# Performance work log

Measured on AMD Instinct MI355X. Metric: run time of the kernel, lower is better.

Reference implementation:

```python
import jax
jax.config.update("jax_enable_x64", True)
import jax.numpy as jnp
import numpy as np

LEAF_VOXEL_SIZE = 0.1
SCALE_UP_FACTOR = 2.0
VOXEL_LEVEL_NUM = 4
BUFFER_SIZE = 4194304
FEATURE_DIM = 8
N_FEATURES = 500000
N_QUERY = 1000000
FEATURE_STD = 0.01

PRIMES = jnp.array([73856093, 19349669, 83492791], dtype=jnp.int64)
# 8 voxel-corner offsets, matching self.steps ordering (z fastest)
STEPS = jnp.array([[0,0,0],[0,0,1],[0,1,0],[0,1,1],[1,0,0],[1,0,1],[1,1,0],[1,1,1]], dtype=jnp.float32)


def setup_inputs() -> dict:
    key = jax.random.key(0)
    k1, k2, k3, k4 = jax.random.split(key, 4)
    # query points spread over a few meters of scene
    query_points = 5.0 * jax.random.normal(k1, (N_QUERY, 3), dtype=jnp.float32)
    features = FEATURE_STD * jax.random.normal(k2, (VOXEL_LEVEL_NUM, N_FEATURES, FEATURE_DIM), dtype=jnp.float32)
    idx = jax.random.randint(k3, (VOXEL_LEVEL_NUM, BUFFER_SIZE), 0, N_FEATURES, dtype=jnp.int64)
    empty = jax.random.uniform(k4, (VOXEL_LEVEL_NUM, BUFFER_SIZE)) < 0.05
    feature_indexs = jnp.where(empty, jnp.int64(-1), idx)
    return {"query_points": query_points, "features": features, "feature_indexs": feature_indexs}


def _interp_coeffs(q, vs):
    # trilinear weights in the same corner order as STEPS -> [N, 8]
    d = q / vs - jnp.floor(q / vs)           # [N,3]
    tx, ty, tz = d[:, 0], d[:, 1], d[:, 2]
    w = jnp.stack([
        (1-tx)*(1-ty)*(1-tz), (1-tx)*(1-ty)*tz, (1-tx)*ty*(1-tz), (1-tx)*ty*tz,
        tx*(1-ty)*(1-tz),     tx*(1-ty)*tz,     tx*ty*(1-tz),     tx*ty*tz,
    ], axis=-1)
    return w


def reference(query_points, features, feature_indexs):
    N = query_points.shape[0]
    sum_features = jnp.zeros((N, FEATURE_DIM), dtype=jnp.float32)
    valid_mask = jnp.ones((N,), dtype=bool)
    for i in range(VOXEL_LEVEL_NUM):
        vs = LEAF_VOXEL_SIZE * SCALE_UP_FACTOR ** i
        grids = jnp.floor(query_points / vs)                       # [N,3]
        corners = (grids[:, None, :] + STEPS).astype(jnp.int64)    # [N,8,3]
        keys = (corners * PRIMES).sum(-1) % BUFFER_SIZE            # [N,8]
        idx = feature_indexs[i][keys]                              # [N,8]
        mask = idx.min(axis=1) >= 0                                # [N]
        safe_idx = jnp.maximum(idx, 0)
        feats = features[i][safe_idx]                              # [N,8,D]
        coeffs = _interp_coeffs(query_points, vs)                  # [N,8]
        contrib = jnp.einsum('ncd,nc->nd', feats, coeffs)          # [N,D]
        sum_features = sum_features + jnp.where(mask[:, None], contrib, 0.0)
        if i == 0:
            valid_mask = mask
    return sum_features, valid_mask
```

## Files before the change

kernel.cpp:

```cpp
#include <hip/hip_runtime.h>

#define BUF_MASK 4194303u
#define BUF_SIZE 4194304
#define NFEAT 500000
#define FDIM 8
#define NLVL 4
#define NBINS 262144
#define NXCD 8

__global__ void detect_int64_kernel(const unsigned int* __restrict__ fi,
                                    int* __restrict__ flag) {
    if (blockIdx.x == 0 && threadIdx.x == 0) {
        int cnt = 0;
        for (int k = 0; k < 128; ++k) {
            unsigned int w = fi[2 * k + 1];
            cnt += (w == 0u || w == 0xFFFFFFFFu) ? 1 : 0;
        }
        *flag = (cnt >= 96) ? 1 : 0;
    }
}

__device__ __forceinline__ unsigned part3(unsigned x) {
    x &= 0x3FFu;
    x = (x | (x << 16)) & 0x030000FFu;
    x = (x | (x << 8))  & 0x0300F00Fu;
    x = (x | (x << 4))  & 0x030C30C3u;
    x = (x | (x << 2))  & 0x09249249u;
    return x;
}

__global__ __launch_bounds__(256) void bin_kernel(
    const float* __restrict__ qp, unsigned* __restrict__ hist,
    unsigned* __restrict__ binA, unsigned* __restrict__ rankA, int N)
{
    int i = blockIdx.x * blockDim.x + threadIdx.x;
    if (i >= N) return;
    float x = qp[3 * (size_t)i + 0];
    float y = qp[3 * (size_t)i + 1];
    float z = qp[3 * (size_t)i + 2];
    int cx = (int)floorf(x * 1.25f) + 32;
    int cy = (int)floorf(y * 1.25f) + 32;
    int cz = (int)floorf(z * 1.25f) + 32;
    cx = min(max(cx, 0), 63); cy = min(max(cy, 0), 63); cz = min(max(cz, 0), 63);
    unsigned m = (part3((unsigned)cx) << 2) | (part3((unsigned)cy) << 1) | part3((unsigned)cz);
    unsigned r = atomicAdd(&hist[m], 1u);
    binA[i] = m; rankA[i] = r;
}

__global__ __launch_bounds__(512) void scan_block(
    const unsigned* __restrict__ hist, unsigned* __restrict__ starts,
    unsigned* __restrict__ bsum)
{
    __shared__ unsigned tmp[512];
    int b = blockIdx.x, t = threadIdx.x;
    unsigned v = hist[(size_t)b * 512 + t];
    tmp[t] = v; __syncthreads();
    for (int o = 1; o < 512; o <<= 1) {
        unsigned add = (t >= o) ? tmp[t - o] : 0u;
        __syncthreads();
        tmp[t] += add;
        __syncthreads();
    }
    starts[(size_t)b * 512 + t] = tmp[t] - v;
    if (t == 511) bsum[b] = tmp[t];
}

__global__ __launch_bounds__(512) void scan_sums(unsigned* __restrict__ bsum) {
    __shared__ unsigned tmp[512];
    int t = threadIdx.x;
    unsigned v = bsum[t];
    tmp[t] = v; __syncthreads();
    for (int o = 1; o < 512; o <<= 1) {
        unsigned add = (t >= o) ? tmp[t - o] : 0u;
        __syncthreads();
        tmp[t] += add;
        __syncthreads();
    }
    bsum[t] = tmp[t] - v;
}

__global__ __launch_bounds__(512) void scan_add(
    unsigned* __restrict__ starts, const unsigned* __restrict__ bsum)
{
    starts[(size_t)blockIdx.x * 512 + threadIdx.x] += bsum[blockIdx.x];
}

__global__ __launch_bounds__(256) void scatter_kernel(
    const float* __restrict__ qp, const unsigned* __restrict__ binA,
    const unsigned* __restrict__ rankA, const unsigned* __restrict__ starts,
    float4* __restrict__ sorted, int N)
{
    int i = blockIdx.x * blockDim.x + threadIdx.x;
    if (i >= N) return;
    unsigned pos = starts[binA[i]] + rankA[i];
    sorted[pos] = make_float4(qp[3 * (size_t)i + 0], qp[3 * (size_t)i + 1],
                              qp[3 * (size_t)i + 2], __uint_as_float((unsigned)i));
}

__global__ __launch_bounds__(256) void nvh_sorted_kernel(
    const float4* __restrict__ sq,
    const float* __restrict__ feats,
    const int*   __restrict__ fidx,
    const int*   __restrict__ flagp,
    float* __restrict__ out,
    int N)
{
    unsigned nwg = gridDim.x, b = blockIdx.x;
    unsigned q = nwg / NXCD, r = nwg % NXCD;
    unsigned xcd = b % NXCD, off = b / NXCD;
    unsigned swz = (xcd < r ? xcd * (q + 1) : r * (q + 1) + (xcd - r) * q) + off;
    int i = (int)(swz * blockDim.x + threadIdx.x);
    if (i >= N) return;
    const int shift = *flagp;

    float4 qv = sq[i];
    float qx = qv.x, qy = qv.y, qz = qv.z;
    unsigned orig = __float_as_uint(qv.w);

    float frx[NLVL], fry[NLVL], frz[NLVL];
    int   idxs[NLVL][8];

    #pragma unroll
    for (int l = 0; l < NLVL; ++l) {
        const float vs = 0.1f * (float)(1 << l);
        float tx = qx / vs, ty = qy / vs, tz = qz / vs;
        float gx = floorf(tx), gy = floorf(ty), gz = floorf(tz);
        frx[l] = tx - gx; fry[l] = ty - gy; frz[l] = tz - gz;
        unsigned h = (unsigned)(int)gx * 73856093u
                   + (unsigned)(int)gy * 19349669u
                   + (unsigned)(int)gz * 83492791u;
        const int* base = fidx + (((size_t)l * BUF_SIZE) << shift);
        #pragma unroll
        for (int c = 0; c < 8; ++c) {
            unsigned key = h;
            if (c & 4) key += 73856093u;
            if (c & 2) key += 19349669u;
            if (c & 1) key += 83492791u;
            key &= BUF_MASK;
            idxs[l][c] = base[(size_t)key << shift];
        }
    }

    float acc[8] = {0.f, 0.f, 0.f, 0.f, 0.f, 0.f, 0.f, 0.f};
    float maskv = 0.0f;

    #pragma unroll
    for (int l = 0; l < NLVL; ++l) {
        int mn = idxs[l][0];
        #pragma unroll
        for (int c = 1; c < 8; ++c) mn = min(mn, idxs[l][c]);
        bool valid = (mn >= 0);
        if (l == 0) maskv = valid ? 1.0f : 0.0f;
        if (valid) {
            const float* fb = feats + (size_t)l * (size_t)NFEAT * FDIM;
            float tx = frx[l], ty = fry[l], tz = frz[l];
            float sx[2] = {1.0f - tx, tx};
            float sy[2] = {1.0f - ty, ty};
            float sz[2] = {1.0f - tz, tz};
            #pragma unroll
            for (int c = 0; c < 8; ++c) {
                float w = (sx[(c >> 2) & 1] * sy[(c >> 1) & 1]) * sz[c & 1];
                const float4* f4 = (const float4*)(fb + (size_t)idxs[l][c] * FDIM);
                float4 a = f4[0];
                float4 b2 = f4[1];
                acc[0] += w * a.x;  acc[1] += w * a.y;
                acc[2] += w * a.z;  acc[3] += w * a.w;
                acc[4] += w * b2.x; acc[5] += w * b2.y;
                acc[6] += w * b2.z; acc[7] += w * b2.w;
            }
        }
    }

    float4* o = (float4*)(out + (size_t)orig * 8);
    o[0] = make_float4(acc[0], acc[1], acc[2], acc[3]);
    o[1] = make_float4(acc[4], acc[5], acc[6], acc[7]);
    out[(size_t)8 * N + orig] = maskv;
}

__global__ __launch_bounds__(256) void nvh_kernel(
    const float* __restrict__ qp, const float* __restrict__ feats,
    const int* __restrict__ fidx, const int* __restrict__ flagp,
    float* __restrict__ out, int N)
{
    int i = blockIdx.x * blockDim.x + threadIdx.x;
    if (i >= N) return;
    const int shift = *flagp;
    float qx = qp[3 * (size_t)i + 0];
    float qy = qp[3 * (size_t)i + 1];
    float qz = qp[3 * (size_t)i + 2];
    float frx[NLVL], fry[NLVL], frz[NLVL];
    int   idxs[NLVL][8];
    #pragma unroll
    for (int l = 0; l < NLVL; ++l) {
        const float vs = 0.1f * (float)(1 << l);
        float tx = qx / vs, ty = qy / vs, tz = qz / vs;
        float gx = floorf(tx), gy = floorf(ty), gz = floorf(tz);
        frx[l] = tx - gx; fry[l] = ty - gy; frz[l] = tz - gz;
        unsigned h = (unsigned)(int)gx * 73856093u
                   + (unsigned)(int)gy * 19349669u
                   + (unsigned)(int)gz * 83492791u;
        const int* base = fidx + (((size_t)l * BUF_SIZE) << shift);
        #pragma unroll
        for (int c = 0; c < 8; ++c) {
            unsigned key = h;
            if (c & 4) key += 73856093u;
            if (c & 2) key += 19349669u;
            if (c & 1) key += 83492791u;
            key &= BUF_MASK;
            idxs[l][c] = base[(size_t)key << shift];
        }
    }
    float acc[8] = {0.f, 0.f, 0.f, 0.f, 0.f, 0.f, 0.f, 0.f};
    float maskv = 0.0f;
    #pragma unroll
    for (int l = 0; l < NLVL; ++l) {
        int mn = idxs[l][0];
        #pragma unroll
        for (int c = 1; c < 8; ++c) mn = min(mn, idxs[l][c]);
        bool valid = (mn >= 0);
        if (l == 0) maskv = valid ? 1.0f : 0.0f;
        if (valid) {
            const float* fb = feats + (size_t)l * (size_t)NFEAT * FDIM;
            float tx = frx[l], ty = fry[l], tz = frz[l];
            float sx[2] = {1.0f - tx, tx};
            float sy[2] = {1.0f - ty, ty};
            float sz[2] = {1.0f - tz, tz};
            #pragma unroll
            for (int c = 0; c < 8; ++c) {
                float w = (sx[(c >> 2) & 1] * sy[(c >> 1) & 1]) * sz[c & 1];
                const float4* f4 = (const float4*)(fb + (size_t)idxs[l][c] * FDIM);
                float4 a = f4[0];
                float4 b2 = f4[1];
                acc[0] += w * a.x;  acc[1] += w * a.y;
                acc[2] += w * a.z;  acc[3] += w * a.w;
                acc[4] += w * b2.x; acc[5] += w * b2.y;
                acc[6] += w * b2.z; acc[7] += w * b2.w;
            }
        }
    }
    float4* o = (float4*)(out + (size_t)i * 8);
    o[0] = make_float4(acc[0], acc[1], acc[2], acc[3]);
    o[1] = make_float4(acc[4], acc[5], acc[6], acc[7]);
    out[(size_t)8 * N + i] = maskv;
}

extern "C" void kernel_launch(void* const* d_in, const int* in_sizes, int n_in,
                              void* d_out, int out_size, void* d_ws, size_t ws_size,
                              hipStream_t stream) {
    const float* qp    = (const float*)d_in[0];
    const float* feats = (const float*)d_in[1];
    const int*   fidx  = (const int*)d_in[2];
    int N = in_sizes[0] / 3;
    int blocks = (N + 255) / 256;

    char* ws = (char*)d_ws;
    size_t off = 0;
    int*      flag   = (int*)(ws + off);      off += 256;
    unsigned* hist   = (unsigned*)(ws + off); off += (size_t)NBINS * 4;
    unsigned* starts = (unsigned*)(ws + off); off += (size_t)NBINS * 4;
    unsigned* bsum   = (unsigned*)(ws + off); off += 512 * 4;
    unsigned* binA   = (unsigned*)(ws + off); off += (size_t)N * 4;
    unsigned* rankA  = (unsigned*)(ws + off); off += (size_t)N * 4;
    off = (off + 15) & ~(size_t)15;
    float4*   sorted = (float4*)(ws + off);   off += (size_t)N * 16;

    detect_int64_kernel<<<1, 64, 0, stream>>>((const unsigned int*)d_in[2], flag);

    if (ws_size < off) {
        nvh_kernel<<<blocks, 256, 0, stream>>>(qp, feats, fidx, flag, (float*)d_out, N);
        return;
    }

    hipMemsetAsync(hist, 0, (size_t)NBINS * 4, stream);
    bin_kernel<<<blocks, 256, 0, stream>>>(qp, hist, binA, rankA, N);
    scan_block<<<512, 512, 0, stream>>>(hist, starts, bsum);
    scan_sums<<<1, 512, 0, stream>>>(bsum);
    scan_add<<<512, 512, 0, stream>>>(starts, bsum);
    scatter_kernel<<<blocks, 256, 0, stream>>>(qp, binA, rankA, starts, sorted, N);
    nvh_sorted_kernel<<<blocks, 256, 0, stream>>>(sorted, feats, fidx, flag, (float*)d_out, N);
}
```

Before: 373.0 us.

## Replace stored bin/rank arrays with atomic cursor scatter and nontemporal memory ops

The binning pass no longer writes per-point bin and rank arrays. The scatter pass recomputes the Morton bin and claims its slot through an atomic increment on a per-bin cursor copied from the exclusive scan. Query reads, sorted-buffer writes and output stores now use nontemporal loads and stores so they do not pollute the cache used by the random feature gathers. This removes about 8 MB of intermediate traffic, but adds a second round of 1M atomics and makes the order of points within a bin nondeterministic.

```diff
diff --git a/kernel.cpp b/kernel.cpp
--- a/kernel.cpp
+++ b/kernel.cpp
@@ -8,6 +8,8 @@
 #define NBINS 262144
 #define NXCD 8
 
+typedef float f4 __attribute__((ext_vector_type(4)));
+
 __global__ void detect_int64_kernel(const unsigned int* __restrict__ fi,
                                     int* __restrict__ flag) {
     if (blockIdx.x == 0 && threadIdx.x == 0) {
@@ -29,27 +31,28 @@
     return x;
 }
 
-__global__ __launch_bounds__(256) void bin_kernel(
-    const float* __restrict__ qp, unsigned* __restrict__ hist,
-    unsigned* __restrict__ binA, unsigned* __restrict__ rankA, int N)
-{
-    int i = blockIdx.x * blockDim.x + threadIdx.x;
-    if (i >= N) return;
-    float x = qp[3 * (size_t)i + 0];
-    float y = qp[3 * (size_t)i + 1];
-    float z = qp[3 * (size_t)i + 2];
+__device__ __forceinline__ unsigned morton_bin(float x, float y, float z) {
     int cx = (int)floorf(x * 1.25f) + 32;
     int cy = (int)floorf(y * 1.25f) + 32;
     int cz = (int)floorf(z * 1.25f) + 32;
     cx = min(max(cx, 0), 63); cy = min(max(cy, 0), 63); cz = min(max(cz, 0), 63);
-    unsigned m = (part3((unsigned)cx) << 2) | (part3((unsigned)cy) << 1) | part3((unsigned)cz);
-    unsigned r = atomicAdd(&hist[m], 1u);
-    binA[i] = m; rankA[i] = r;
+    return (part3((unsigned)cx) << 2) | (part3((unsigned)cy) << 1) | part3((unsigned)cz);
+}
+
+__global__ __launch_bounds__(256) void hist_kernel(
+    const float* __restrict__ qp, unsigned* __restrict__ hist, int N)
+{
+    int i = blockIdx.x * blockDim.x + threadIdx.x;
+    if (i >= N) return;
+    float x = __builtin_nontemporal_load(qp + 3 * (size_t)i + 0);
+    float y = __builtin_nontemporal_load(qp + 3 * (size_t)i + 1);
+    float z = __builtin_nontemporal_load(qp + 3 * (size_t)i + 2);
+    atomicAdd(&hist[morton_bin(x, y, z)], 1u);
 }
 
 __global__ __launch_bounds__(512) void scan_block(
     const unsigned* __restrict__ hist, unsigned* __restrict__ starts,
-    unsigned* __restrict__ bsum)
+    unsigned* __restrict__ cursor, unsigned* __restrict__ bsum)
 {
     __shared__ unsigned tmp[512];
     int b = blockIdx.x, t = threadIdx.x;
@@ -61,7 +64,9 @@
         tmp[t] += add;
         __syncthreads();
     }
-    starts[(size_t)b * 512 + t] = tmp[t] - v;
+    unsigned ex = tmp[t] - v;
+    starts[(size_t)b * 512 + t] = ex;
+    cursor[(size_t)b * 512 + t] = ex;
     if (t == 511) bsum[b] = tmp[t];
 }
 
@@ -80,25 +85,32 @@
 }
 
 __global__ __launch_bounds__(512) void scan_add(
-    unsigned* __restrict__ starts, const unsigned* __restrict__ bsum)
-{
-    starts[(size_t)blockIdx.x * 512 + threadIdx.x] += bsum[blockIdx.x];
+    unsigned* __restrict__ starts, unsigned* __restrict__ cursor,
+    const unsigned* __restrict__ bsum)
+{
+    unsigned add = bsum[blockIdx.x];
+    size_t p = (size_t)blockIdx.x * 512 + threadIdx.x;
+    starts[p] += add;
+    cursor[p] += add;
 }
 
 __global__ __launch_bounds__(256) void scatter_kernel(
-    const float* __restrict__ qp, const unsigned* __restrict__ binA,
-    const unsigned* __restrict__ rankA, const unsigned* __restrict__ starts,
-    float4* __restrict__ sorted, int N)
+    const float* __restrict__ qp, unsigned* __restrict__ cursor,
+    f4* __restrict__ sorted, int N)
 {
     int i = blockIdx.x * blockDim.x + threadIdx.x;
     if (i >= N) return;
-    unsigned pos = starts[binA[i]] + rankA[i];
-    sorted[pos] = make_float4(qp[3 * (size_t)i + 0], qp[3 * (size_t)i + 1],
-                              qp[3 * (size_t)i + 2], __uint_as_float((unsigned)i));
+    float x = __builtin_nontemporal_load(qp + 3 * (size_t)i + 0);
+    float y = __builtin_nontemporal_load(qp + 3 * (size_t)i + 1);
+    float z = __builtin_nontemporal_load(qp + 3 * (size_t)i + 2);
+    unsigned m = morton_bin(x, y, z);
+    unsigned pos = atomicAdd(&cursor[m], 1u);
+    f4 v = {x, y, z, __uint_as_float((unsigned)i)};
+    __builtin_nontemporal_store(v, sorted + pos);
 }
 
 __global__ __launch_bounds__(256) void nvh_sorted_kernel(
-    const float4* __restrict__ sq,
+    const f4* __restrict__ sq,
     const float* __restrict__ feats,
     const int*   __restrict__ fidx,
     const int*   __restrict__ flagp,
@@ -113,7 +125,7 @@
     if (i >= N) return;
     const int shift = *flagp;
 
-    float4 qv = sq[i];
+    f4 qv = __builtin_nontemporal_load(sq + i);
     float qx = qv.x, qy = qv.y, qz = qv.z;
     unsigned orig = __float_as_uint(qv.w);
 
@@ -160,9 +172,9 @@
             #pragma unroll
             for (int c = 0; c < 8; ++c) {
                 float w = (sx[(c >> 2) & 1] * sy[(c >> 1) & 1]) * sz[c & 1];
-                const float4* f4 = (const float4*)(fb + (size_t)idxs[l][c] * FDIM);
-                float4 a = f4[0];
-                float4 b2 = f4[1];
+                const float4* f4p = (const float4*)(fb + (size_t)idxs[l][c] * FDIM);
+                float4 a = f4p[0];
+                float4 b2 = f4p[1];
                 acc[0] += w * a.x;  acc[1] += w * a.y;
                 acc[2] += w * a.z;  acc[3] += w * a.w;
                 acc[4] += w * b2.x; acc[5] += w * b2.y;
@@ -171,10 +183,12 @@
         }
     }
 
-    float4* o = (float4*)(out + (size_t)orig * 8);
-    o[0] = make_float4(acc[0], acc[1], acc[2], acc[3]);
-    o[1] = make_float4(acc[4], acc[5], acc[6], acc[7]);
-    out[(size_t)8 * N + orig] = maskv;
+    f4 o0 = {acc[0], acc[1], acc[2], acc[3]};
+    f4 o1 = {acc[4], acc[5], acc[6], acc[7]};
+    f4* op = (f4*)(out + (size_t)orig * 8);
+    __builtin_nontemporal_store(o0, op);
+    __builtin_nontemporal_store(o1, op + 1);
+    __builtin_nontemporal_store(maskv, out + (size_t)8 * N + orig);
 }
 
 __global__ __launch_bounds__(256) void nvh_kernel(
@@ -228,9 +242,9 @@
             #pragma unroll
             for (int c = 0; c < 8; ++c) {
                 float w = (sx[(c >> 2) & 1] * sy[(c >> 1) & 1]) * sz[c & 1];
-                const float4* f4 = (const float4*)(fb + (size_t)idxs[l][c] * FDIM);
-                float4 a = f4[0];
-                float4 b2 = f4[1];
+                const float4* f4p = (const float4*)(fb + (size_t)idxs[l][c] * FDIM);
+                float4 a = f4p[0];
+                float4 b2 = f4p[1];
                 acc[0] += w * a.x;  acc[1] += w * a.y;
                 acc[2] += w * a.z;  acc[3] += w * a.w;
                 acc[4] += w * b2.x; acc[5] += w * b2.y;
@@ -258,11 +272,10 @@
     int*      flag   = (int*)(ws + off);      off += 256;
     unsigned* hist   = (unsigned*)(ws + off); off += (size_t)NBINS * 4;
     unsigned* starts = (unsigned*)(ws + off); off += (size_t)NBINS * 4;
+    unsigned* cursor = (unsigned*)(ws + off); off += (size_t)NBINS * 4;
     unsigned* bsum   = (unsigned*)(ws + off); off += 512 * 4;
-    unsigned* binA   = (unsigned*)(ws + off); off += (size_t)N * 4;
-    unsigned* rankA  = (unsigned*)(ws + off); off += (size_t)N * 4;
     off = (off + 15) & ~(size_t)15;
-    float4*   sorted = (float4*)(ws + off);   off += (size_t)N * 16;
+    f4*       sorted = (f4*)(ws + off);       off += (size_t)N * 16;
 
     detect_int64_kernel<<<1, 64, 0, stream>>>((const unsigned int*)d_in[2], flag);
 
@@ -272,10 +285,10 @@
     }
 
     hipMemsetAsync(hist, 0, (size_t)NBINS * 4, stream);
-    bin_kernel<<<blocks, 256, 0, stream>>>(qp, hist, binA, rankA, N);
-    scan_block<<<512, 512, 0, stream>>>(hist, starts, bsum);
+    hist_kernel<<<blocks, 256, 0, stream>>>(qp, hist, N);
+    scan_block<<<512, 512, 0, stream>>>(hist, starts, cursor, bsum);
     scan_sums<<<1, 512, 0, stream>>>(bsum);
-    scan_add<<<512, 512, 0, stream>>>(starts, bsum);
-    scatter_kernel<<<blocks, 256, 0, stream>>>(qp, binA, rankA, starts, sorted, N);
+    scan_add<<<512, 512, 0, stream>>>(starts, cursor, bsum);
+    scatter_kernel<<<blocks, 256, 0, stream>>>(qp, cursor, sorted, N);
     nvh_sorted_kernel<<<blocks, 256, 0, stream>>>(sorted, feats, fidx, flag, (float*)d_out, N);
 }
```

Result: slower. 439.4 us (+17.8%).

## Deduplicate voxel-corner lookups per block via shared-memory bounding-box cache

Applied to the files above, without the earlier changes.

Replaces the sorted per-query kernel with a 512-thread kernel that reduces each block's grid-coordinate bounding box per level. When the box holds at most 2048 cells, the block cooperatively loads each cell's hash index and feature once into shared memory, and queries then interpolate from shared memory. Features are stored in shared memory as fp16 to fit the cache, which adds rounding error to the outputs. Blocks whose box is too large fall back to the original direct gathers. The change aims to cut redundant random global gathers among spatially sorted neighbouring queries, at the cost of extra block synchronisation and bounding-box reduction work.

```diff
diff --git a/kernel.cpp b/kernel.cpp
--- a/kernel.cpp
+++ b/kernel.cpp
@@ -1,4 +1,5 @@
 #include <hip/hip_runtime.h>
+#include <limits.h>
 
 #define BUF_MASK 4194303u
 #define BUF_SIZE 4194304
@@ -7,6 +8,10 @@
 #define NLVL 4
 #define NBINS 262144
 #define NXCD 8
+#define CAP 2048
+
+typedef float f4 __attribute__((ext_vector_type(4)));
+typedef _Float16 h8 __attribute__((ext_vector_type(8)));
 
 __global__ void detect_int64_kernel(const unsigned int* __restrict__ fi,
                                     int* __restrict__ flag) {
@@ -97,84 +102,168 @@
                               qp[3 * (size_t)i + 2], __uint_as_float((unsigned)i));
 }
 
-__global__ __launch_bounds__(256) void nvh_sorted_kernel(
-    const float4* __restrict__ sq,
+__global__ __launch_bounds__(512) void nvh_dedup(
+    const f4* __restrict__ sq,
     const float* __restrict__ feats,
     const int*   __restrict__ fidx,
     const int*   __restrict__ flagp,
     float* __restrict__ out,
     int N)
 {
+    __shared__ int s_idx[CAP];
+    __shared__ h8  s_feat[CAP];
+    __shared__ int s_red[8][6];
+
     unsigned nwg = gridDim.x, b = blockIdx.x;
     unsigned q = nwg / NXCD, r = nwg % NXCD;
-    unsigned xcd = b % NXCD, off = b / NXCD;
-    unsigned swz = (xcd < r ? xcd * (q + 1) : r * (q + 1) + (xcd - r) * q) + off;
+    unsigned xcd = b % NXCD, offb = b / NXCD;
+    unsigned swz = (xcd < r ? xcd * (q + 1) : r * (q + 1) + (xcd - r) * q) + offb;
     int i = (int)(swz * blockDim.x + threadIdx.x);
-    if (i >= N) return;
+    bool active = (i < N);
     const int shift = *flagp;
-
-    float4 qv = sq[i];
+    int tid = threadIdx.x, wid = tid >> 6;
+
+    f4 qv = {0.f, 0.f, 0.f, 0.f};
+    if (active) qv = sq[i];
     float qx = qv.x, qy = qv.y, qz = qv.z;
     unsigned orig = __float_as_uint(qv.w);
 
-    float frx[NLVL], fry[NLVL], frz[NLVL];
-    int   idxs[NLVL][8];
-
-    #pragma unroll
+    float acc[8] = {0.f, 0.f, 0.f, 0.f, 0.f, 0.f, 0.f, 0.f};
+    float maskv = 0.0f;
+
     for (int l = 0; l < NLVL; ++l) {
         const float vs = 0.1f * (float)(1 << l);
         float tx = qx / vs, ty = qy / vs, tz = qz / vs;
-        float gx = floorf(tx), gy = floorf(ty), gz = floorf(tz);
-        frx[l] = tx - gx; fry[l] = ty - gy; frz[l] = tz - gz;
-        unsigned h = (unsigned)(int)gx * 73856093u
-                   + (unsigned)(int)gy * 19349669u
-                   + (unsigned)(int)gz * 83492791u;
+        float gxf = floorf(tx), gyf = floorf(ty), gzf = floorf(tz);
+        float fx = tx - gxf, fy = ty - gyf, fz = tz - gzf;
+        int gx = (int)gxf, gy = (int)gyf, gz = (int)gzf;
+
+        int a0 = active ? gx : INT_MAX, a1 = active ? gy : INT_MAX, a2 = active ? gz : INT_MAX;
+        int b0 = active ? gx : INT_MIN, b1 = active ? gy : INT_MIN, b2 = active ? gz : INT_MIN;
+        #pragma unroll
+        for (int o = 32; o; o >>= 1) {
+            a0 = min(a0, __shfl_xor(a0, o)); b0 = max(b0, __shfl_xor(b0, o));
+            a1 = min(a1, __shfl_xor(a1, o)); b1 = max(b1, __shfl_xor(b1, o));
+            a2 = min(a2, __shfl_xor(a2, o)); b2 = max(b2, __shfl_xor(b2, o));
+        }
+        __syncthreads();
+        if ((tid & 63) == 0) {
+            s_red[wid][0] = a0; s_red[wid][1] = a1; s_red[wid][2] = a2;
+            s_red[wid][3] = b0; s_red[wid][4] = b1; s_red[wid][5] = b2;
+        }
+        __syncthreads();
+        int mnx = s_red[0][0], mny = s_red[0][1], mnz = s_red[0][2];
+        int mxx = s_red[0][3], mxy = s_red[0][4], mxz = s_red[0][5];
+        #pragma unroll
+        for (int w = 1; w < 8; ++w) {
+            mnx = min(mnx, s_red[w][0]); mny = min(mny, s_red[w][1]); mnz = min(mnz, s_red[w][2]);
+            mxx = max(mxx, s_red[w][3]); mxy = max(mxy, s_red[w][4]); mxz = max(mxz, s_red[w][5]);
+        }
+
+        int dx = mxx - mnx + 2, dy = mxy - mny + 2, dz = mxz - mnz + 2;
+        long long T = (long long)dx * dy * dz;
         const int* base = fidx + (((size_t)l * BUF_SIZE) << shift);
-        #pragma unroll
-        for (int c = 0; c < 8; ++c) {
-            unsigned key = h;
-            if (c & 4) key += 73856093u;
-            if (c & 2) key += 19349669u;
-            if (c & 1) key += 83492791u;
-            key &= BUF_MASK;
-            idxs[l][c] = base[(size_t)key << shift];
-        }
-    }
-
-    float acc[8] = {0.f, 0.f, 0.f, 0.f, 0.f, 0.f, 0.f, 0.f};
-    float maskv = 0.0f;
-
-    #pragma unroll
-    for (int l = 0; l < NLVL; ++l) {
-        int mn = idxs[l][0];
-        #pragma unroll
-        for (int c = 1; c < 8; ++c) mn = min(mn, idxs[l][c]);
-        bool valid = (mn >= 0);
-        if (l == 0) maskv = valid ? 1.0f : 0.0f;
-        if (valid) {
-            const float* fb = feats + (size_t)l * (size_t)NFEAT * FDIM;
-            float tx = frx[l], ty = fry[l], tz = frz[l];
-            float sx[2] = {1.0f - tx, tx};
-            float sy[2] = {1.0f - ty, ty};
-            float sz[2] = {1.0f - tz, tz};
-            #pragma unroll
-            for (int c = 0; c < 8; ++c) {
-                float w = (sx[(c >> 2) & 1] * sy[(c >> 1) & 1]) * sz[c & 1];
-                const float4* f4 = (const float4*)(fb + (size_t)idxs[l][c] * FDIM);
-                float4 a = f4[0];
-                float4 b2 = f4[1];
-                acc[0] += w * a.x;  acc[1] += w * a.y;
-                acc[2] += w * a.z;  acc[3] += w * a.w;
-                acc[4] += w * b2.x; acc[5] += w * b2.y;
-                acc[6] += w * b2.z; acc[7] += w * b2.w;
+        const float* fb = feats + (size_t)l * (size_t)NFEAT * FDIM;
+
+        if (T <= (long long)CAP) {
+            int Ti = (int)T;
+            for (int t = tid; t < Ti; t += 512) {
+                int ox = t % dx, rem = t / dx;
+                int oy = rem % dy, oz = rem / dy;
+                unsigned h = (unsigned)(mnx + ox) * 73856093u
+                           + (unsigned)(mny + oy) * 19349669u
+                           + (unsigned)(mnz + oz) * 83492791u;
+                int id = base[(size_t)(h & BUF_MASK) << shift];
+                s_idx[t] = id;
+                if (id >= 0) {
+                    const f4* fp = (const f4*)(fb + (size_t)id * FDIM);
+                    f4 va = fp[0], vb = fp[1];
+                    h8 hv;
+                    hv[0] = (_Float16)va.x; hv[1] = (_Float16)va.y;
+                    hv[2] = (_Float16)va.z; hv[3] = (_Float16)va.w;
+                    hv[4] = (_Float16)vb.x; hv[5] = (_Float16)vb.y;
+                    hv[6] = (_Float16)vb.z; hv[7] = (_Float16)vb.w;
+                    s_feat[t] = hv;
+                }
             }
-        }
-    }
-
-    float4* o = (float4*)(out + (size_t)orig * 8);
-    o[0] = make_float4(acc[0], acc[1], acc[2], acc[3]);
-    o[1] = make_float4(acc[4], acc[5], acc[6], acc[7]);
-    out[(size_t)8 * N + orig] = maskv;
+            __syncthreads();
+            if (active) {
+                int bx = gx - mnx, by = gy - mny, bz = gz - mnz;
+                int offs[8], idxs[8];
+                #pragma unroll
+                for (int c = 0; c < 8; ++c) {
+                    int off = (bx + ((c >> 2) & 1))
+                            + dx * ((by + ((c >> 1) & 1)) + dy * (bz + (c & 1)));
+                    offs[c] = off;
+                    idxs[c] = s_idx[off];
+                }
+                int mn = idxs[0];
+                #pragma unroll
+                for (int c = 1; c < 8; ++c) mn = min(mn, idxs[c]);
+                bool valid = (mn >= 0);
+                if (l == 0) maskv = valid ? 1.0f : 0.0f;
+                if (valid) {
+                    float sx[2] = {1.0f - fx, fx};
+                    float sy[2] = {1.0f - fy, fy};
+                    float sz[2] = {1.0f - fz, fz};
+                    #pragma unroll
+                    for (int c = 0; c < 8; ++c) {
+                        float w = (sx[(c >> 2) & 1] * sy[(c >> 1) & 1]) * sz[c & 1];
+                        h8 v = s_feat[offs[c]];
+                        acc[0] += w * (float)v[0]; acc[1] += w * (float)v[1];
+                        acc[2] += w * (float)v[2]; acc[3] += w * (float)v[3];
+                        acc[4] += w * (float)v[4]; acc[5] += w * (float)v[5];
+                        acc[6] += w * (float)v[6]; acc[7] += w * (float)v[7];
+                    }
+                }
+            }
+        } else {
+            if (active) {
+                unsigned h = (unsigned)gx * 73856093u
+                           + (unsigned)gy * 19349669u
+                           + (unsigned)gz * 83492791u;
+                int idxs[8];
+                #pragma unroll
+                for (int c = 0; c < 8; ++c) {
+                    unsigned key = h;
+                    if (c & 4) key += 73856093u;
+                    if (c & 2) key += 19349669u;
+                    if (c & 1) key += 83492791u;
+                    key &= BUF_MASK;
+                    idxs[c] = base[(size_t)key << shift];
+                }
+                int mn = idxs[0];
+                #pragma unroll
+                for (int c = 1; c < 8; ++c) mn = min(mn, idxs[c]);
+                bool valid = (mn >= 0);
+                if (l == 0) maskv = valid ? 1.0f : 0.0f;
+                if (valid) {
+                    float sx[2] = {1.0f - fx, fx};
+                    float sy[2] = {1.0f - fy, fy};
+                    float sz[2] = {1.0f - fz, fz};
+                    #pragma unroll
+                    for (int c = 0; c < 8; ++c) {
+                        float w = (sx[(c >> 2) & 1] * sy[(c >> 1) & 1]) * sz[c & 1];
+                        const f4* f4p = (const f4*)(fb + (size_t)idxs[c] * FDIM);
+                        f4 va = f4p[0], vb = f4p[1];
+                        acc[0] += w * va.x; acc[1] += w * va.y;
+                        acc[2] += w * va.z; acc[3] += w * va.w;
+                        acc[4] += w * vb.x; acc[5] += w * vb.y;
+                        acc[6] += w * vb.z; acc[7] += w * vb.w;
+                    }
+                }
+            }
+        }
+    }
+
+    if (active) {
+        f4 o0 = {acc[0], acc[1], acc[2], acc[3]};
+        f4 o1 = {acc[4], acc[5], acc[6], acc[7]};
+        f4* op = (f4*)(out + (size_t)orig * 8);
+        op[0] = o0;
+        op[1] = o1;
+        out[(size_t)8 * N + orig] = maskv;
+    }
 }
 
 __global__ __launch_bounds__(256) void nvh_kernel(
@@ -228,9 +317,9 @@
             #pragma unroll
             for (int c = 0; c < 8; ++c) {
                 float w = (sx[(c >> 2) & 1] * sy[(c >> 1) & 1]) * sz[c & 1];
-                const float4* f4 = (const float4*)(fb + (size_t)idxs[l][c] * FDIM);
-                float4 a = f4[0];
-                float4 b2 = f4[1];
+                const f4* f4p = (const f4*)(fb + (size_t)idxs[l][c] * FDIM);
+                f4 a = f4p[0];
+                f4 b2 = f4p[1];
                 acc[0] += w * a.x;  acc[1] += w * a.y;
                 acc[2] += w * a.z;  acc[3] += w * a.w;
                 acc[4] += w * b2.x; acc[5] += w * b2.y;
@@ -252,6 +341,7 @@
     const int*   fidx  = (const int*)d_in[2];
     int N = in_sizes[0] / 3;
     int blocks = (N + 255) / 256;
+    int blocks512 = (N + 511) / 512;
 
     char* ws = (char*)d_ws;
     size_t off = 0;
@@ -263,10 +353,11 @@
     unsigned* rankA  = (unsigned*)(ws + off); off += (size_t)N * 4;
     off = (off + 15) & ~(size_t)15;
     float4*   sorted = (float4*)(ws + off);   off += (size_t)N * 16;
+    size_t need_sort = off;
 
     detect_int64_kernel<<<1, 64, 0, stream>>>((const unsigned int*)d_in[2], flag);
 
-    if (ws_size < off) {
+    if (ws_size < need_sort) {
         nvh_kernel<<<blocks, 256, 0, stream>>>(qp, feats, fidx, flag, (float*)d_out, N);
         return;
     }
@@ -277,5 +368,5 @@
     scan_sums<<<1, 512, 0, stream>>>(bsum);
     scan_add<<<512, 512, 0, stream>>>(starts, bsum);
     scatter_kernel<<<blocks, 256, 0, stream>>>(qp, binA, rankA, starts, sorted, N);
-    nvh_sorted_kernel<<<blocks, 256, 0, stream>>>(sorted, feats, fidx, flag, (float*)d_out, N);
-}
+    nvh_dedup<<<blocks512, 512, 0, stream>>>((const f4*)sorted, feats, fidx, flag, (float*)d_out, N);
+}
```

After: 402.6 us. +7.9%, slower.
